# Performance work log

Measured on AMD Instinct MI355X. Metric: run time of the kernel, lower is better.

Reference implementation:

```python
import jax, jax.numpy as jnp
import numpy as np

# Physics constants from SpinOrbitConfig / module body
ALPHA = 0.02            # rashba_strength
BETA = 0.015            # dresselhaus_strength
E_EX = 0.1              # exchange_energy
ZEEMAN = 5.79e-5 * 2.0 * 0.1   # mu_B * g * zeeman_field
T_EVO = 1e-11           # phase_coherence_time
HBAR = 6.582e-16
SCALE = T_EVO / HBAR    # ~1.519e4
DEPH = 1e7 * T_EVO      # dephasing_rate * evolution_time = 1e-4
PI = np.pi


def _expm2x2(m00, m01, m10, m11):
    """Closed-form exp of batched 2x2 complex matrices (elements are (B,) arrays).
    exp(M) = e^mu (cosh(d) I + sinh(d)/d * (M - mu I)), mu = tr/2, d^2 = a^2 + m01*m10."""
    mu = 0.5 * (m00 + m11)
    a = m00 - mu                      # M - mu*I has diag (a, -a)
    delta = jnp.sqrt(a * a + m01 * m10)
    small = jnp.abs(delta) < 1e-12
    dsafe = jnp.where(small, jnp.ones_like(delta), delta)
    sinhc = jnp.where(small, jnp.ones_like(delta), jnp.sinh(dsafe) / dsafe)
    c = jnp.cosh(delta)
    e = jnp.exp(mu)
    return e * (c + sinhc * a), e * sinhc * m01, e * sinhc * m10, e * (c - sinhc * a)


def setup_inputs() -> dict:
    B, D = 1048576, 16
    k0, k1, k2, k3 = jax.random.split(jax.random.key(0), 4)
    return {
        "input_data": jax.random.normal(k0, (B, D), jnp.float32),
        "spinor_re": jax.random.normal(k1, (B, 2), jnp.float32),
        "spinor_im": jax.random.normal(k2, (B, 2), jnp.float32),
        "exchange_fields": 0.1 * jax.random.normal(k3, (D, 3), jnp.float32),
        "topological_gap": jnp.full((1,), 1e-3, jnp.float32),
    }


def reference(input_data, spinor_re, spinor_im, exchange_fields, topological_gap):
    # ---- initialize normalized spinor (hoisted randn -> inputs) ----
    psi0 = (spinor_re + 1j * spinor_im).astype(jnp.complex64)   # (B,2)
    psi0 = psi0 / jnp.sqrt(jnp.sum(jnp.abs(psi0) ** 2, axis=1, keepdims=True))

    # ---- spin-orbit Hamiltonian (combined Rashba + Dresselhaus + exchange + Zeeman + gap) ----
    kx = input_data[:, 0]
    ky = input_data[:, 1]
    J = jnp.mean(exchange_fields, axis=0)   # (3,)
    hx = ALPHA * ky + BETA * kx + E_EX * J[0]            # coeff of sigma_x
    hy = -ALPHA * kx - BETA * ky + E_EX * J[1]           # coeff of sigma_y
    hz = E_EX * J[2] + ZEEMAN + topological_gap[0]       # coeff of sigma_z
    hz = jnp.broadcast_to(hz, kx.shape)
    # H = [[hz, hx - i hy], [hx + i hy, -hz]]
    H00 = hz.astype(jnp.complex64)
    H11 = (-hz).astype(jnp.complex64)
    H01 = (hx - 1j * hy).astype(jnp.complex64)
    H10 = (hx + 1j * hy).astype(jnp.complex64)

    # ---- evolution: U = exp(-i (H - i*DEPH*I) * T/hbar) ----
    jscale = jnp.complex64(-1j * SCALE)
    damp = jnp.complex64(-SCALE * DEPH)   # from -i * (-i*DEPH*I) * SCALE
    u00, u01, u10, u11 = _expm2x2(jscale * H00 + damp, jscale * H01,
                                  jscale * H10, jscale * H11 + damp)
    p0 = u00 * psi0[:, 0] + u01 * psi0[:, 1]
    p1 = u10 * psi0[:, 0] + u11 * psi0[:, 1]
    psi = jnp.stack([p0, p1], axis=1)     # (B,2) evolved state

    # ---- Berry phase ----
    phases = jnp.angle(psi)
    bp = jnp.mean(phases[:, 1] - phases[:, 0])
    berry_phase = (bp + PI) % (2 * PI) - PI

    # ---- spin polarization / classical output ----
    cross = p0 * jnp.conj(p1)
    sx = jnp.real(cross + jnp.conj(cross))
    sy = jnp.real(-1j * (cross - jnp.conj(cross)))
    sz = jnp.abs(p0) ** 2 - jnp.abs(p1) ** 2
    output = jnp.stack([sx, sy, sz], axis=1)   # (B,3)

    # ---- topological charge (winding of in-plane spin over batch sequence) ----
    ang = jnp.arctan2(sy, sx)
    dang = ang[1:] - ang[:-1]
    dang = (dang + PI) % (2 * PI) - PI
    charge = jnp.round(jnp.sum(dang) / (2 * PI)).astype(jnp.int32)

    momentum = input_data[:, :2]
    return output, psi, momentum, berry_phase, charge
```

## Files before the change

kernel.cpp:

```cpp
#include <hip/hip_runtime.h>
#include <math.h>

#define ALPHA_F   0.02f
#define BETA_F    0.015f
#define E_EX_F    0.1f
#define ZEEMAN_F  (5.79e-05f * 2.0f * 0.1f)
#define SCALE_F   ((float)(1e-11 / 6.582e-16))
#define DEPH_F    1e-4f

typedef float vf2 __attribute__((ext_vector_type(2)));
typedef float vf4 __attribute__((ext_vector_type(4)));

__global__ __launch_bounds__(256) void main_k(
    const float* __restrict__ inp,
    const float* __restrict__ sre,
    const float* __restrict__ sim,
    const float* __restrict__ exf,
    const float* __restrict__ gap,
    float* __restrict__ out, long long out_size,
    double* __restrict__ blkB, double* __restrict__ blkD,
    float2* __restrict__ firstS, float2* __restrict__ lastS,
    int chunk, long long B, int Dex)
{
    const int t = threadIdx.x;
    const long long base = (long long)blockIdx.x * chunk;
    const int ntile = chunk >> 8;

    vf2 k_c  = __builtin_nontemporal_load((const vf2*)(inp + (base + t) * 16));
    vf2 re_c = __builtin_nontemporal_load((const vf2*)(sre + (base + t) * 2));
    vf2 im_c = __builtin_nontemporal_load((const vf2*)(sim + (base + t) * 2));

    float j0 = 0.f, j1 = 0.f, j2 = 0.f;
    for (int d = 0; d < Dex; ++d) { j0 += exf[d*3]; j1 += exf[d*3+1]; j2 += exf[d*3+2]; }
    const float invD = 1.f / (float)Dex;
    const float cx  = E_EX_F * (j0 * invD);
    const float cy  = E_EX_F * (j1 * invD);
    const float hzc = E_EX_F * (j2 * invD) + ZEEMAN_F + gap[0];
    const float Ef  = expf(-SCALE_F * DEPH_F);

    const long long psi_off = 3 * B;
    const long long mom_off = 7 * B;

    __shared__ float  sS[768];
    __shared__ float2 sFirst[4];
    __shared__ float2 sCarry[2];
    __shared__ double rr1[4], rr2[4];

    double v1 = 0.0, v2 = 0.0;
    float2 zlast = make_float2(0.f, 0.f);
    const int wid = t >> 6, lane = t & 63;

    for (int tile = 0; tile < ntile; ++tile) {
        const long long icur = base + (long long)tile * 256 + t;
        const vf2 k = k_c, re = re_c, im = im_c;

        if (tile + 1 < ntile) {
            const long long inx = icur + 256;
            k_c  = __builtin_nontemporal_load((const vf2*)(inp + inx * 16));
            re_c = __builtin_nontemporal_load((const vf2*)(sre + inx * 2));
            im_c = __builtin_nontemporal_load((const vf2*)(sim + inx * 2));
        }

        const float nrm = re.x*re.x + re.y*re.y + im.x*im.x + im.y*im.y;
        const float inv = rsqrtf(nrm);
        const float a0r = re.x*inv, a0i = im.x*inv;
        const float a1r = re.y*inv, a1i = im.y*inv;

        const float hx = ALPHA_F*k.y + BETA_F*k.x + cx;
        const float hy = -ALPHA_F*k.x - BETA_F*k.y + cy;

        const float r = sqrtf(hx*hx + hy*hy + hzc*hzc);
        float s, c;
        __sincosf(SCALE_F * r, &s, &c);
        const float f  = Ef * s / fmaxf(r, 1e-37f);
        const float Ec = Ef * c;
        const float fz = f*hzc, fx = f*hx, fy = f*hy;

        const float p0r = Ec*a0r + fz*a0i - fy*a1r + fx*a1i;
        const float p0i = Ec*a0i - fz*a0r - fy*a1i - fx*a1r;
        const float p1r = Ec*a1r - fz*a1i + fy*a0r + fx*a0i;
        const float p1i = Ec*a1i + fz*a1r + fy*a0i - fx*a0r;

        const float crr = p0r*p1r + p0i*p1i;
        const float cri = p0i*p1r - p0r*p1i;
        const float sx = 2.f*crr, sy = 2.f*cri;
        const float sz = (p0r*p0r + p0i*p0i) - (p1r*p1r + p1i*p1i);

        const long long o4 = psi_off + icur * 4;
        if (o4 + 3 < out_size) {
            vf4 pv = {p0r, p0i, p1r, p1i};
            __builtin_nontemporal_store(pv, (vf4*)(out + o4));
        }
        const long long o2 = mom_off + icur * 2;
        if (o2 + 1 < out_size) {
            vf2 mv = {k.x, k.y};
            __builtin_nontemporal_store(mv, (vf2*)(out + o2));
        }

        sS[t*3 + 0] = sx; sS[t*3 + 1] = sy; sS[t*3 + 2] = sz;
        if (lane == 0)  sFirst[wid] = make_float2(sx, sy);
        if (t == 255)   sCarry[tile & 1] = make_float2(sx, sy);

        const float znx = __shfl_down(sx, 1);
        const float zny = __shfl_down(sy, 1);
        __syncthreads();

        const long long tb3 = (base + (long long)tile * 256) * 3;
        if (tb3 + 767 < out_size) {
            __builtin_nontemporal_store(sS[t],       out + tb3 + t);
            __builtin_nontemporal_store(sS[256 + t], out + tb3 + 256 + t);
            __builtin_nontemporal_store(sS[512 + t], out + tb3 + 512 + t);
        } else {
            if (tb3 + t < out_size)       out[tb3 + t]       = sS[t];
            if (tb3 + 256 + t < out_size) out[tb3 + 256 + t] = sS[256 + t];
            if (tb3 + 512 + t < out_size) out[tb3 + 512 + t] = sS[512 + t];
        }

        v1 += (double)(atan2f(p1i, p1r) - atan2f(p0i, p0r));

        if (lane < 63) {
            const float dot = znx*sx + zny*sy;
            const float crs = sx*zny - sy*znx;
            v2 += (double)atan2f(crs, dot);
        } else if (wid < 3) {
            const float2 nf = sFirst[wid + 1];
            const float dot = nf.x*sx + nf.y*sy;
            const float crs = sx*nf.y - sy*nf.x;
            v2 += (double)atan2f(crs, dot);
        }
        if (t == 0) {
            if (tile > 0) {
                const float2 pz = sCarry[(tile & 1) ^ 1];
                const float dot = sx*pz.x + sy*pz.y;
                const float crs = pz.x*sy - pz.y*sx;
                v2 += (double)atan2f(crs, dot);
            } else {
                firstS[blockIdx.x] = make_float2(sx, sy);
            }
        }
        if (t == 255) zlast = make_float2(sx, sy);
        __syncthreads();
    }
    if (t == 255) lastS[blockIdx.x] = zlast;

    for (int o = 32; o; o >>= 1) { v1 += __shfl_down(v1, o); v2 += __shfl_down(v2, o); }
    if (lane == 0) { rr1[wid] = v1; rr2[wid] = v2; }
    __syncthreads();
    if (t == 0) {
        blkB[blockIdx.x] = rr1[0] + rr1[1] + rr1[2] + rr1[3];
        blkD[blockIdx.x] = rr2[0] + rr2[1] + rr2[2] + rr2[3];
    }
}

__global__ __launch_bounds__(256) void final_k(
    const double* __restrict__ blkB, const double* __restrict__ blkD,
    const float2* __restrict__ firstS, const float2* __restrict__ lastS,
    int nblk, long long B, float* __restrict__ out, long long out_size)
{
    const int t = threadIdx.x;
    double s1 = 0.0, s2 = 0.0;
    for (int b = t; b < nblk; b += 256) { s1 += blkB[b]; s2 += blkD[b]; }
    for (int b = t; b < nblk - 1; b += 256) {
        const float2 a = lastS[b], f2 = firstS[b + 1];
        const float dot = f2.x*a.x + f2.y*a.y;
        const float crs = a.x*f2.y - a.y*f2.x;
        s2 += (double)atan2f(crs, dot);
    }
    for (int o = 32; o; o >>= 1) { s1 += __shfl_down(s1, o); s2 += __shfl_down(s2, o); }
    __shared__ double rr1[4], rr2[4];
    const int wid = t >> 6, lane = t & 63;
    if (lane == 0) { rr1[wid] = s1; rr2[wid] = s2; }
    __syncthreads();
    if (t == 0 && out_size >= 2) {
        const double sum_dph  = rr1[0] + rr1[1] + rr1[2] + rr1[3];
        const double sum_dang = rr2[0] + rr2[1] + rr2[2] + rr2[3];
        double bp = sum_dph / (double)B;
        double w = fmod(bp + (double)M_PI, 2.0 * (double)M_PI);
        if (w < 0.0) w += 2.0 * (double)M_PI;
        out[out_size - 2] = (float)(w - (double)M_PI);
        out[out_size - 1] = (float)nearbyint(sum_dang / (2.0 * (double)M_PI));
    }
}

extern "C" void kernel_launch(void* const* d_in, const int* in_sizes, int n_in,
                              void* d_out, int out_size, void* d_ws, size_t ws_size,
                              hipStream_t stream) {
    (void)n_in;
    const float* inp = (const float*)d_in[0];
    const float* sre = (const float*)d_in[1];
    const float* sim = (const float*)d_in[2];
    const float* exf = (const float*)d_in[3];
    const float* gap = (const float*)d_in[4];

    const long long B   = (long long)in_sizes[0] / 16;
    const int       Dex = in_sizes[3] / 3;

    int nblk = 64;
    const int cands[6] = {2048, 1024, 512, 256, 128, 64};
    for (int ci = 0; ci < 6; ++ci) {
        const int c = cands[ci];
        if (B % ((long long)c * 256) == 0 && (size_t)c * 32 + 64 <= ws_size) {
            nblk = c;
            break;
        }
    }
    const int chunk = (int)(B / nblk);

    char* ws = (char*)d_ws;
    double*  blkB   = (double*)(ws);
    double*  blkD   = (double*)(ws + (size_t)nblk * 8);
    float2*  firstS = (float2*)(ws + (size_t)nblk * 16);
    float2*  lastS  = (float2*)(ws + (size_t)nblk * 24);

    main_k<<<nblk, 256, 0, stream>>>(inp, sre, sim, exf, gap,
                                     (float*)d_out, (long long)out_size,
                                     blkB, blkD, firstS, lastS,
                                     chunk, B, Dex);
    final_k<<<1, 256, 0, stream>>>(blkB, blkD, firstS, lastS,
                                   nblk, B, (float*)d_out, (long long)out_size);
}
```

Before: 30.77 us.

## Process two 256-element tiles per iteration and vectorize spin output stores

The main loop now handles 512 elements per iteration, with each thread processing two elements. All six input loads for the pair are issued up front, replacing the one-tile-ahead register prefetch. Neighbour angle differences now read from shared memory instead of shuffles plus per-wave first values, and the (B,3) spin output is written with float4 nontemporal stores. This halves the number of barrier-separated iterations and widens the stores. In exchange it drops cross-iteration prefetching and raises register pressure, and block-size selection now requires B to divide by 512 per block.

```diff
diff --git a/kernel.cpp b/kernel.cpp
--- a/kernel.cpp
+++ b/kernel.cpp
@@ -24,122 +24,136 @@
 {
     const int t = threadIdx.x;
     const long long base = (long long)blockIdx.x * chunk;
-    const int ntile = chunk >> 8;
-
-    vf2 k_c  = __builtin_nontemporal_load((const vf2*)(inp + (base + t) * 16));
-    vf2 re_c = __builtin_nontemporal_load((const vf2*)(sre + (base + t) * 2));
-    vf2 im_c = __builtin_nontemporal_load((const vf2*)(sim + (base + t) * 2));
-
-    float j0 = 0.f, j1 = 0.f, j2 = 0.f;
-    for (int d = 0; d < Dex; ++d) { j0 += exf[d*3]; j1 += exf[d*3+1]; j2 += exf[d*3+2]; }
+    const int npair = chunk >> 9;
+
+    float j0 = 0.f, j1s = 0.f, j2 = 0.f;
+    for (int d = 0; d < Dex; ++d) { j0 += exf[d*3]; j1s += exf[d*3+1]; j2 += exf[d*3+2]; }
     const float invD = 1.f / (float)Dex;
     const float cx  = E_EX_F * (j0 * invD);
-    const float cy  = E_EX_F * (j1 * invD);
+    const float cy  = E_EX_F * (j1s * invD);
     const float hzc = E_EX_F * (j2 * invD) + ZEEMAN_F + gap[0];
     const float Ef  = expf(-SCALE_F * DEPH_F);
 
     const long long psi_off = 3 * B;
     const long long mom_off = 7 * B;
 
-    __shared__ float  sS[768];
-    __shared__ float2 sFirst[4];
-    __shared__ float2 sCarry[2];
+    __shared__ __align__(16) float sS[1536];
+    __shared__ float2 sCarryP[2];
     __shared__ double rr1[4], rr2[4];
 
     double v1 = 0.0, v2 = 0.0;
     float2 zlast = make_float2(0.f, 0.f);
     const int wid = t >> 6, lane = t & 63;
 
-    for (int tile = 0; tile < ntile; ++tile) {
-        const long long icur = base + (long long)tile * 256 + t;
-        const vf2 k = k_c, re = re_c, im = im_c;
-
-        if (tile + 1 < ntile) {
-            const long long inx = icur + 256;
-            k_c  = __builtin_nontemporal_load((const vf2*)(inp + inx * 16));
-            re_c = __builtin_nontemporal_load((const vf2*)(sre + inx * 2));
-            im_c = __builtin_nontemporal_load((const vf2*)(sim + inx * 2));
-        }
-
-        const float nrm = re.x*re.x + re.y*re.y + im.x*im.x + im.y*im.y;
-        const float inv = rsqrtf(nrm);
-        const float a0r = re.x*inv, a0i = im.x*inv;
-        const float a1r = re.y*inv, a1i = im.y*inv;
-
-        const float hx = ALPHA_F*k.y + BETA_F*k.x + cx;
-        const float hy = -ALPHA_F*k.x - BETA_F*k.y + cy;
-
-        const float r = sqrtf(hx*hx + hy*hy + hzc*hzc);
-        float s, c;
-        __sincosf(SCALE_F * r, &s, &c);
-        const float f  = Ef * s / fmaxf(r, 1e-37f);
-        const float Ec = Ef * c;
-        const float fz = f*hzc, fx = f*hx, fy = f*hy;
-
-        const float p0r = Ec*a0r + fz*a0i - fy*a1r + fx*a1i;
-        const float p0i = Ec*a0i - fz*a0r - fy*a1i - fx*a1r;
-        const float p1r = Ec*a1r - fz*a1i + fy*a0r + fx*a0i;
-        const float p1i = Ec*a1i + fz*a1r + fy*a0i - fx*a0r;
-
-        const float crr = p0r*p1r + p0i*p1i;
-        const float cri = p0i*p1r - p0r*p1i;
-        const float sx = 2.f*crr, sy = 2.f*cri;
-        const float sz = (p0r*p0r + p0i*p0i) - (p1r*p1r + p1i*p1i);
-
-        const long long o4 = psi_off + icur * 4;
-        if (o4 + 3 < out_size) {
-            vf4 pv = {p0r, p0i, p1r, p1i};
-            __builtin_nontemporal_store(pv, (vf4*)(out + o4));
-        }
-        const long long o2 = mom_off + icur * 2;
-        if (o2 + 1 < out_size) {
-            vf2 mv = {k.x, k.y};
-            __builtin_nontemporal_store(mv, (vf2*)(out + o2));
-        }
-
-        sS[t*3 + 0] = sx; sS[t*3 + 1] = sy; sS[t*3 + 2] = sz;
-        if (lane == 0)  sFirst[wid] = make_float2(sx, sy);
-        if (t == 255)   sCarry[tile & 1] = make_float2(sx, sy);
-
-        const float znx = __shfl_down(sx, 1);
-        const float zny = __shfl_down(sy, 1);
+    for (int pair = 0; pair < npair; ++pair) {
+        const long long pb = base + (long long)pair * 512;
+        const long long i0 = pb + t;
+        const long long i1 = pb + 256 + t;
+
+        if (pair > 0) __syncthreads();
+
+        const vf2 k0  = __builtin_nontemporal_load((const vf2*)(inp + i0 * 16));
+        const vf2 k1  = __builtin_nontemporal_load((const vf2*)(inp + i1 * 16));
+        const vf2 re0 = __builtin_nontemporal_load((const vf2*)(sre + i0 * 2));
+        const vf2 re1 = __builtin_nontemporal_load((const vf2*)(sre + i1 * 2));
+        const vf2 im0 = __builtin_nontemporal_load((const vf2*)(sim + i0 * 2));
+        const vf2 im1 = __builtin_nontemporal_load((const vf2*)(sim + i1 * 2));
+
+        float zx[2], zy[2];
+
+        #pragma unroll
+        for (int j = 0; j < 2; ++j) {
+            const vf2 k  = j ? k1  : k0;
+            const vf2 re = j ? re1 : re0;
+            const vf2 im = j ? im1 : im0;
+            const long long i = j ? i1 : i0;
+
+            const float nrm = re.x*re.x + re.y*re.y + im.x*im.x + im.y*im.y;
+            const float inv = rsqrtf(nrm);
+            const float a0r = re.x*inv, a0i = im.x*inv;
+            const float a1r = re.y*inv, a1i = im.y*inv;
+
+            const float hx = ALPHA_F*k.y + BETA_F*k.x + cx;
+            const float hy = -ALPHA_F*k.x - BETA_F*k.y + cy;
+
+            const float r = sqrtf(hx*hx + hy*hy + hzc*hzc);
+            float s, c;
+            __sincosf(SCALE_F * r, &s, &c);
+            const float f  = Ef * s / fmaxf(r, 1e-37f);
+            const float Ec = Ef * c;
+            const float fz = f*hzc, fx = f*hx, fy = f*hy;
+
+            const float p0r = Ec*a0r + fz*a0i - fy*a1r + fx*a1i;
+            const float p0i = Ec*a0i - fz*a0r - fy*a1i - fx*a1r;
+            const float p1r = Ec*a1r - fz*a1i + fy*a0r + fx*a0i;
+            const float p1i = Ec*a1i + fz*a1r + fy*a0i - fx*a0r;
+
+            const float crr = p0r*p1r + p0i*p1i;
+            const float cri = p0i*p1r - p0r*p1i;
+            const float sx = 2.f*crr, sy = 2.f*cri;
+            const float sz = (p0r*p0r + p0i*p0i) - (p1r*p1r + p1i*p1i);
+
+            const long long o4 = psi_off + i * 4;
+            if (o4 + 3 < out_size) {
+                vf4 pv = {p0r, p0i, p1r, p1i};
+                __builtin_nontemporal_store(pv, (vf4*)(out + o4));
+            }
+            const long long o2 = mom_off + i * 2;
+            if (o2 + 1 < out_size) {
+                vf2 mv = {k.x, k.y};
+                __builtin_nontemporal_store(mv, (vf2*)(out + o2));
+            }
+
+            const int li = j * 256 + t;
+            sS[li*3 + 0] = sx; sS[li*3 + 1] = sy; sS[li*3 + 2] = sz;
+
+            v1 += (double)(atan2f(p1i, p1r) - atan2f(p0i, p0r));
+            zx[j] = sx; zy[j] = sy;
+        }
+
         __syncthreads();
 
-        const long long tb3 = (base + (long long)tile * 256) * 3;
-        if (tb3 + 767 < out_size) {
-            __builtin_nontemporal_store(sS[t],       out + tb3 + t);
-            __builtin_nontemporal_store(sS[256 + t], out + tb3 + 256 + t);
-            __builtin_nontemporal_store(sS[512 + t], out + tb3 + 512 + t);
+        const long long tb3 = pb * 3;
+        if (tb3 + 1535 < out_size) {
+            const int x0 = t * 4;
+            vf4 a = {sS[x0], sS[x0+1], sS[x0+2], sS[x0+3]};
+            __builtin_nontemporal_store(a, (vf4*)(out + tb3 + x0));
+            if (t < 128) {
+                const int x1 = 1024 + t * 4;
+                vf4 b = {sS[x1], sS[x1+1], sS[x1+2], sS[x1+3]};
+                __builtin_nontemporal_store(b, (vf4*)(out + tb3 + x1));
+            }
         } else {
-            if (tb3 + t < out_size)       out[tb3 + t]       = sS[t];
-            if (tb3 + 256 + t < out_size) out[tb3 + 256 + t] = sS[256 + t];
-            if (tb3 + 512 + t < out_size) out[tb3 + 512 + t] = sS[512 + t];
-        }
-
-        v1 += (double)(atan2f(p1i, p1r) - atan2f(p0i, p0r));
-
-        if (lane < 63) {
-            const float dot = znx*sx + zny*sy;
-            const float crs = sx*zny - sy*znx;
+            for (int q = t; q < 1536; q += 256)
+                if (tb3 + q < out_size) out[tb3 + q] = sS[q];
+        }
+
+        {
+            const float nx = sS[(t+1)*3], ny = sS[(t+1)*3 + 1];
+            const float dot = nx*zx[0] + ny*zy[0];
+            const float crs = zx[0]*ny - zy[0]*nx;
             v2 += (double)atan2f(crs, dot);
-        } else if (wid < 3) {
-            const float2 nf = sFirst[wid + 1];
-            const float dot = nf.x*sx + nf.y*sy;
-            const float crs = sx*nf.y - sy*nf.x;
+        }
+        if (t < 255) {
+            const float nx = sS[(257+t)*3], ny = sS[(257+t)*3 + 1];
+            const float dot = nx*zx[1] + ny*zy[1];
+            const float crs = zx[1]*ny - zy[1]*nx;
             v2 += (double)atan2f(crs, dot);
         }
         if (t == 0) {
-            if (tile > 0) {
-                const float2 pz = sCarry[(tile & 1) ^ 1];
-                const float dot = sx*pz.x + sy*pz.y;
-                const float crs = pz.x*sy - pz.y*sx;
+            if (pair > 0) {
+                const float2 pz = sCarryP[(pair & 1) ^ 1];
+                const float dot = zx[0]*pz.x + zy[0]*pz.y;
+                const float crs = pz.x*zy[0] - pz.y*zx[0];
                 v2 += (double)atan2f(crs, dot);
             } else {
-                firstS[blockIdx.x] = make_float2(sx, sy);
-            }
-        }
-        if (t == 255) zlast = make_float2(sx, sy);
-        __syncthreads();
+                firstS[blockIdx.x] = make_float2(zx[0], zy[0]);
+            }
+        }
+        if (t == 255) {
+            sCarryP[pair & 1] = make_float2(zx[1], zy[1]);
+            zlast = make_float2(zx[1], zy[1]);
+        }
     }
     if (t == 255) lastS[blockIdx.x] = zlast;
 
@@ -199,7 +213,7 @@
     const int cands[6] = {2048, 1024, 512, 256, 128, 64};
     for (int ci = 0; ci < 6; ++ci) {
         const int c = cands[ci];
-        if (B % ((long long)c * 256) == 0 && (size_t)c * 32 + 64 <= ws_size) {
+        if (B % ((long long)c * 512) == 0 && (size_t)c * 32 + 64 <= ws_size) {
             nblk = c;
             break;
         }
```

Result: no change. 31.14 us (+1.2%).
